# Kernel optimization log

Hardware: AMD Instinct MI355X
Metric: run time of the kernel (lower is better)

The kernel has to match this reference:

```python
import jax, jax.numpy as jnp
import numpy as np

B, N, D, S, H = 64, 4096, 256, 8, 256
ITERS = 3
EPS = 1e-8
SCALE = D ** -0.5


def _ln(x, g, b):
    m = jnp.mean(x, axis=-1, keepdims=True)
    v = jnp.mean((x - m) ** 2, axis=-1, keepdims=True)
    return (x - m) * jax.lax.rsqrt(v + 1e-5) * g + b


def setup_inputs() -> dict:
    key = jax.random.key(0)
    ks = jax.random.split(key, 12)
    s = 0.02
    return {
        'inputs': jax.random.normal(ks[0], (B, N, D), jnp.float32),
        'slot_noise': jax.random.normal(ks[1], (B, S, D), jnp.float32),
        'slots_mean': jax.random.normal(ks[2], (1, 1, D), jnp.float32),
        'slots_logvar': s * jax.random.normal(ks[3], (1, 1, D), jnp.float32),
        'Wq': s * jax.random.normal(ks[4], (D, D), jnp.float32),
        'bq': jnp.zeros((D,), jnp.float32),
        'Wk': s * jax.random.normal(ks[5], (D, D), jnp.float32),
        'bk': jnp.zeros((D,), jnp.float32),
        'Wv': s * jax.random.normal(ks[6], (D, D), jnp.float32),
        'bv': jnp.zeros((D,), jnp.float32),
        'W_ih': s * jax.random.normal(ks[7], (3 * D, D), jnp.float32),
        'b_ih': jnp.zeros((3 * D,), jnp.float32),
        'W_hh': s * jax.random.normal(ks[8], (3 * D, D), jnp.float32),
        'b_hh': jnp.zeros((3 * D,), jnp.float32),
        'W1': s * jax.random.normal(ks[9], (H, D), jnp.float32),
        'b1': jnp.zeros((H,), jnp.float32),
        'W2': s * jax.random.normal(ks[10], (D, H), jnp.float32),
        'b2': jnp.zeros((D,), jnp.float32),
        'g_in': jnp.ones((D,), jnp.float32),
        'bias_in': jnp.zeros((D,), jnp.float32),
        'g_slots': jnp.ones((D,), jnp.float32),
        'bias_slots': jnp.zeros((D,), jnp.float32),
        'g_ff': jnp.ones((D,), jnp.float32),
        'bias_ff': jnp.zeros((D,), jnp.float32),
    }


def reference(inputs, slot_noise, slots_mean, slots_logvar, Wq, bq, Wk, bk, Wv, bv,
              W_ih, b_ih, W_hh, b_hh, W1, b1, W2, b2,
              g_in, bias_in, g_slots, bias_slots, g_ff, bias_ff):
    # slot init: mean + exp(logvar) * noise  (exp(logvar) used as multiplier, as in source)
    slots = slots_mean + jnp.exp(slots_logvar) * slot_noise  # [B,S,D]
    x = _ln(inputs, g_in, bias_in)                            # [B,N,D]
    k = x @ Wk.T + bk
    v = x @ Wv.T + bv
    attn = None
    for _ in range(ITERS):
        slots_prev = slots
        sn = _ln(slots, g_slots, bias_slots)
        q = sn @ Wq.T + bq                                    # [B,S,D]
        dots = jnp.einsum('bid,bjd->bij', q, k) * SCALE       # [B,S,N]
        attn = jax.nn.softmax(dots, axis=1) + EPS             # softmax over slots, no renorm
        updates = jnp.einsum('bjd,bij->bid', v, attn)         # [B,S,D]
        # GRUCell (PyTorch convention)
        gi = updates @ W_ih.T + b_ih                          # [B,S,3D]
        gh = slots_prev @ W_hh.T + b_hh
        i_r, i_z, i_n = jnp.split(gi, 3, axis=-1)
        h_r, h_z, h_n = jnp.split(gh, 3, axis=-1)
        r = jax.nn.sigmoid(i_r + h_r)
        z = jax.nn.sigmoid(i_z + h_z)
        n = jnp.tanh(i_n + r * h_n)
        slots = (1.0 - z) * n + z * slots_prev
        # MLP residual
        sf = _ln(slots, g_ff, bias_ff)
        slots = slots + (jax.nn.relu(sf @ W1.T + b1) @ W2.T + b2)
    return (slots, attn)
```

## Files before the change

### kernel.cpp

```cpp
#include <hip/hip_runtime.h>

typedef unsigned short u16;
typedef __bf16 bf16x8 __attribute__((ext_vector_type(8)));
typedef float f32x4 __attribute__((ext_vector_type(4)));
typedef float f32x2 __attribute__((ext_vector_type(2)));

#define DEV static __device__ __forceinline__

DEV u16 f2bf(float f) {
    unsigned int u = __builtin_bit_cast(unsigned int, f);
    u += 0x7FFFu + ((u >> 16) & 1u);
    return (u16)(u >> 16);
}

DEV bf16x8 frag_ld(const u16* p) {
    return __builtin_bit_cast(bf16x8, *(const uint4*)p);
}

DEV float sigm(float x) { return 1.f / (1.f + __expf(-x)); }

DEV float blo(unsigned u) { return __builtin_bit_cast(float, u << 16); }
DEV float bhi(unsigned u) { return __builtin_bit_cast(float, u & 0xffff0000u); }
DEV f32x2 bf2(unsigned u) { return (f32x2){ blo(u), bhi(u) }; }

DEV int sw(int row, int colu16) { return row * 256 + (colu16 ^ ((row & 7) << 3)); }

DEV void gld16(const u16* g, u16* l) {
    __builtin_amdgcn_global_load_lds(
        (const __attribute__((address_space(1))) unsigned int*)g,
        (__attribute__((address_space(3))) unsigned int*)l, 16, 0, 0);
}

__global__ __launch_bounds__(256) void kSetupLN(
    const float* __restrict__ X, const float* __restrict__ gin, const float* __restrict__ bin,
    u16* __restrict__ XN,
    const float* __restrict__ noise, const float* __restrict__ mean,
    const float* __restrict__ logv, float* __restrict__ slots,
    const float* __restrict__ Wq, const float* __restrict__ Wk,
    const float* __restrict__ bq, const float* __restrict__ bk,
    float* __restrict__ Wqk, float* __restrict__ wbc,
    const float* __restrict__ Wv,  float* __restrict__ WvT,
    const float* __restrict__ Wih, float* __restrict__ WihT,
    const float* __restrict__ Whh, float* __restrict__ WhhT,
    const float* __restrict__ W1,  float* __restrict__ W1T,
    const float* __restrict__ W2,  float* __restrict__ W2T)
{
    __shared__ float tile[32][33];
    const int bid = blockIdx.x, t = threadIdx.x;
    if (bid < 2048) {
        const int w = t >> 6, lane = t & 63;
        const int c = lane << 2;
        const float4 g4 = *(const float4*)(gin + c);
        const float4 b4 = *(const float4*)(bin + c);
        const size_t r0 = (size_t)bid * 128 + (size_t)w * 32;
        #pragma unroll 4
        for (int i = 0; i < 32; ++i) {
            const float4 x = *(const float4*)(X + (r0 + i) * 256 + c);
            float s1 = x.x + x.y + x.z + x.w;
            float s2 = x.x * x.x + x.y * x.y + x.z * x.z + x.w * x.w;
            #pragma unroll
            for (int o = 32; o > 0; o >>= 1) { s1 += __shfl_xor(s1, o); s2 += __shfl_xor(s2, o); }
            const float mu = s1 * (1.f / 256.f);
            const float rs = rsqrtf(s2 * (1.f / 256.f) - mu * mu + 1e-5f);
            ushort4 pk;
            pk.x = f2bf((x.x - mu) * rs * g4.x + b4.x);
            pk.y = f2bf((x.y - mu) * rs * g4.y + b4.y);
            pk.z = f2bf((x.z - mu) * rs * g4.z + b4.z);
            pk.w = f2bf((x.w - mu) * rs * g4.w + b4.w);
            *(ushort4*)(XN + (r0 + i) * 256 + c) = pk;
        }
        return;
    }
    if (bid < 2560) {
        const int id = (bid - 2048) * 256 + t;
        const int d = id & 255;
        slots[id] = mean[d] + __expf(logv[d]) * noise[id];
        return;
    }
    if (bid < 2818) {
        const int a = bid - 2560, e = t;
        if (a < 256) {
            float acc = 0.f;
            for (int d = 0; d < 256; ++d) acc += Wq[(size_t)d * 256 + a] * Wk[(size_t)d * 256 + e];
            Wqk[(size_t)a * 256 + e] = acc;
        } else if (a == 256) {
            float acc = 0.f;
            for (int d = 0; d < 256; ++d) acc += bq[d] * Wk[(size_t)d * 256 + e];
            wbc[e] = acc;
        } else {
            float acc = 0.f;
            for (int d = 0; d < 256; ++d) acc += Wq[(size_t)d * 256 + e] * bk[d];
            wbc[256 + e] = acc;
            if (e == 0) {
                float c0 = 0.f;
                for (int d = 0; d < 256; ++d) c0 += bq[d] * bk[d];
                wbc[512] = c0;
            }
        }
        return;
    }
    const int rb = bid - 2818;
    const float* in; float* outp; int R, k;
    if (rb < 64)       { in = Wv;  outp = WvT;  R = 256; k = rb; }
    else if (rb < 256) { in = Wih; outp = WihT; R = 768; k = rb - 64; }
    else if (rb < 448) { in = Whh; outp = WhhT; R = 768; k = rb - 256; }
    else if (rb < 512) { in = W1;  outp = W1T;  R = 256; k = rb - 448; }
    else               { in = W2;  outp = W2T;  R = 256; k = rb - 512; }
    const int bx = k & 7, by = k >> 3;
    const int tx = t & 31, ty = t >> 5;
    const int c0 = bx * 32, r0 = by * 32;
    #pragma unroll
    for (int i = 0; i < 4; ++i)
        tile[ty + i * 8][tx] = in[(size_t)(r0 + ty + i * 8) * 256 + c0 + tx];
    __syncthreads();
    #pragma unroll
    for (int i = 0; i < 4; ++i)
        outp[(size_t)(c0 + ty + i * 8) * R + r0 + tx] = tile[tx][ty + i * 8];
}

__global__ __launch_bounds__(256) void kSn(
    const float* __restrict__ slots, const float* __restrict__ gs, const float* __restrict__ bs,
    const float* __restrict__ Wqk, const float* __restrict__ wbc,
    u16* __restrict__ qo, float* __restrict__ qc)
{
    __shared__ float SN[8][256];
    __shared__ float red2[4][8][64];
    const int t = threadIdx.x;
    const int b = blockIdx.y, seg = blockIdx.x;
    const int w = t >> 6, lane = t & 63;
    #pragma unroll
    for (int rr = 0; rr < 2; ++rr) {
        const int r = w * 2 + rr;
        const int c = lane * 4;
        const float4 x = *(const float4*)(slots + ((size_t)b * 8 + r) * 256 + c);
        float s1 = x.x + x.y + x.z + x.w;
        float s2 = x.x * x.x + x.y * x.y + x.z * x.z + x.w * x.w;
        #pragma unroll
        for (int o = 32; o > 0; o >>= 1) { s1 += __shfl_xor(s1, o); s2 += __shfl_xor(s2, o); }
        const float mu = s1 * (1.f / 256.f);
        const float rs = rsqrtf(s2 * (1.f / 256.f) - mu * mu + 1e-5f);
        const float4 g4 = *(const float4*)(gs + c);
        const float4 b4 = *(const float4*)(bs + c);
        SN[r][c + 0] = (x.x - mu) * rs * g4.x + b4.x;
        SN[r][c + 1] = (x.y - mu) * rs * g4.y + b4.y;
        SN[r][c + 2] = (x.z - mu) * rs * g4.z + b4.z;
        SN[r][c + 3] = (x.w - mu) * rs * g4.w + b4.w;
    }
    __syncthreads();
    const int c = seg * 64 + (t & 63);
    const int p = t >> 6;
    float acc[8] = {};
    #pragma unroll 4
    for (int d = p * 64; d < p * 64 + 64; ++d) {
        const float wq = Wqk[(size_t)d * 256 + c];
        #pragma unroll
        for (int r = 0; r < 8; ++r) acc[r] += wq * SN[r][d];
    }
    #pragma unroll
    for (int r = 0; r < 8; ++r) red2[p][r][t & 63] = acc[r];
    __syncthreads();
    const float bb = wbc[c];
    #pragma unroll
    for (int rr = t >> 6; rr < 8; rr += 4) {
        const float s = red2[0][rr][t & 63] + red2[1][rr][t & 63]
                      + red2[2][rr][t & 63] + red2[3][rr][t & 63];
        qo[((size_t)b * 16 + rr) * 256 + c] = f2bf((s + bb) * 0.0625f);
    }
    if (seg == 0) {
        const int r = t >> 5, l = t & 31;
        float a = 0.f;
        #pragma unroll
        for (int d8 = 0; d8 < 8; ++d8) a += SN[r][l * 8 + d8] * wbc[256 + l * 8 + d8];
        #pragma unroll
        for (int o = 16; o > 0; o >>= 1) a += __shfl_xor(a, o);
        if (l == 0) qc[(size_t)b * 8 + r] = 0.0625f * (a + wbc[512]);
    }
}

__global__ __launch_bounds__(256, 3) void kF(
    const u16* __restrict__ Q,
    const float* __restrict__ qcg,
    const u16* __restrict__ XN,
    float* __restrict__ attn_out,
    float* __restrict__ part,
    float* __restrict__ part2,
    int write_attn)
{
    __shared__ __align__(16) u16 stash[2 * 64 * 256];
    __shared__ __align__(16) float att32[64][8];
    const int tid = threadIdx.x;
    const int w = tid >> 6, lane = tid & 63;
    const int quad = lane >> 4, l16 = lane & 15;
    const int dsg = lane & 31, jg = lane >> 5;
    const int qb1 = (quad & 1) << 2;
    const int b = blockIdx.y, nt = blockIdx.x;
    const int j0 = nt << 8;
    const size_t rowbase = (size_t)b * 4096 + j0;
    const int srow = w * 16;

    const u16* qptr = Q + (size_t)b * 16 * 256;
    bf16x8 qfrag[8];
    #pragma unroll
    for (int k0 = 0; k0 < 8; ++k0)
        qfrag[k0] = frag_ld(qptr + l16 * 256 + k0 * 32 + quad * 8);

    float c8[8];
    #pragma unroll
    for (int i = 0; i < 8; ++i) c8[i] = qcg[(size_t)b * 8 + i];

    f32x2 acc2[8][4];
    #pragma unroll
    for (int i = 0; i < 8; ++i)
        #pragma unroll
        for (int k = 0; k < 4; ++k) acc2[i][k] = (f32x2){0.f, 0.f};
    float sacc[4] = {};

#define STAGE(ck, h)                                                          \
    {                                                                         \
        const u16* xb = XN + (rowbase + (ck) * 64) * 256;                     \
        u16* dst = stash + (h) * 16384;                                       \
        _Pragma("unroll")                                                     \
        for (int i = 0; i < 8; ++i) {                                         \
            const int il = i * 64 + lane;                                     \
            const int rloc = il >> 5;                                         \
            const int ug = (il & 31) ^ (rloc & 7);                            \
            gld16(xb + (size_t)(srow + rloc) * 256 + ug * 8,                  \
                  dst + ((srow << 5) + il) * 8);                              \
        }                                                                     \
    }

    STAGE(0, 0);
    for (int st = 0; st < 4; ++st) {
        if (st < 3) {
            STAGE(st + 1, (st + 1) & 1);
            asm volatile("s_waitcnt vmcnt(8)" ::: "memory");
        } else {
            asm volatile("s_waitcnt vmcnt(0)" ::: "memory");
        }
        const u16* sh = stash + (st & 1) * 16384;
        __builtin_amdgcn_s_setprio(1);

        f32x4 dacc = {};
        #pragma unroll
        for (int k0 = 0; k0 < 8; ++k0) {
            const bf16x8 bfr = frag_ld(sh + sw(srow + l16, k0 * 32 + quad * 8));
            dacc = __builtin_amdgcn_mfma_f32_16x16x32_bf16(qfrag[k0], bfr, dacc, 0, 0, 0);
        }
        {
            float v[8];
            #pragma unroll
            for (int r = 0; r < 4; ++r) {
                v[qb1 + r]       = dacc[r];
                v[(qb1 ^ 4) + r] = __shfl_xor(dacc[r], 16);
            }
            #pragma unroll
            for (int i = 0; i < 8; ++i) v[i] += c8[i];
            float m = v[0];
            #pragma unroll
            for (int i = 1; i < 8; ++i) m = fmaxf(m, v[i]);
            float s = 0.f;
            #pragma unroll
            for (int i = 0; i < 8; ++i) { v[i] = __expf(v[i] - m); s += v[i]; }
            const float inv = 1.f / s;
            if (quad < 2) {
                float4 av;
                av.x = v[qb1 + 0] * inv + 1e-8f;
                av.y = v[qb1 + 1] * inv + 1e-8f;
                av.z = v[qb1 + 2] * inv + 1e-8f;
                av.w = v[qb1 + 3] * inv + 1e-8f;
                sacc[0] += av.x; sacc[1] += av.y; sacc[2] += av.z; sacc[3] += av.w;
                *(float4*)&att32[srow + l16][qb1] = av;
                if (write_attn) {
                    const size_t jglob = j0 + st * 64 + srow + l16;
                    attn_out[((size_t)b * 8 + qb1 + 0) * 4096 + jglob] = av.x;
                    attn_out[((size_t)b * 8 + qb1 + 1) * 4096 + jglob] = av.y;
                    attn_out[((size_t)b * 8 + qb1 + 2) * 4096 + jglob] = av.z;
                    attn_out[((size_t)b * 8 + qb1 + 3) * 4096 + jglob] = av.w;
                }
            }
        }
        #pragma unroll
        for (int jj = 0; jj < 8; ++jj) {
            const int row = srow + jj * 2 + jg;
            const uint4 raw = *(const uint4*)(sh + sw(row, dsg * 8));
            const float4 a0 = *(const float4*)&att32[row][0];
            const float4 a1 = *(const float4*)&att32[row][4];
            f32x2 xf[4];
            xf[0] = bf2(raw.x); xf[1] = bf2(raw.y); xf[2] = bf2(raw.z); xf[3] = bf2(raw.w);
            const float av8[8] = {a0.x, a0.y, a0.z, a0.w, a1.x, a1.y, a1.z, a1.w};
            #pragma unroll
            for (int i = 0; i < 8; ++i) {
                const f32x2 aa = (f32x2){av8[i], av8[i]};
                #pragma unroll
                for (int k = 0; k < 4; ++k)
                    acc2[i][k] = aa * xf[k] + acc2[i][k];
            }
        }
        __builtin_amdgcn_s_setprio(0);
    }
#undef STAGE

    #pragma unroll
    for (int i = 0; i < 8; ++i)
        #pragma unroll
        for (int k = 0; k < 4; ++k) {
            acc2[i][k][0] += __shfl_xor(acc2[i][k][0], 32);
            acc2[i][k][1] += __shfl_xor(acc2[i][k][1], 32);
        }
    #pragma unroll
    for (int r = 0; r < 4; ++r)
        #pragma unroll
        for (int o = 1; o < 16; o <<= 1) sacc[r] += __shfl_xor(sacc[r], o);

    __syncthreads();
    float* usred = (float*)stash;
    float* sred2 = (float*)att32;
    if (jg == 0) {
        #pragma unroll
        for (int i = 0; i < 8; ++i) {
            float4 lo, hi;
            lo.x = acc2[i][0][0]; lo.y = acc2[i][0][1]; lo.z = acc2[i][1][0]; lo.w = acc2[i][1][1];
            hi.x = acc2[i][2][0]; hi.y = acc2[i][2][1]; hi.z = acc2[i][3][0]; hi.w = acc2[i][3][1];
            *(float4*)&usred[(w * 8 + i) * 256 + dsg * 8]     = lo;
            *(float4*)&usred[(w * 8 + i) * 256 + dsg * 8 + 4] = hi;
        }
    }
    if (l16 == 0 && quad < 2) {
        #pragma unroll
        for (int r = 0; r < 4; ++r) sred2[(w * 2 + quad) * 4 + r] = sacc[r];
    }
    __syncthreads();
    const size_t pb = ((size_t)nt * 64 + b) * 8;
    #pragma unroll
    for (int i = 0; i < 8; ++i) {
        const float s = usred[(0 * 8 + i) * 256 + tid] + usred[(1 * 8 + i) * 256 + tid]
                      + usred[(2 * 8 + i) * 256 + tid] + usred[(3 * 8 + i) * 256 + tid];
        part[(pb + i) * 256 + tid] = s;
    }
    if (tid < 8) {
        const int q = tid >> 2, r = tid & 3;
        part2[pb + tid] = sred2[(0 * 2 + q) * 4 + r] + sred2[(1 * 2 + q) * 4 + r]
                        + sred2[(2 * 2 + q) * 4 + r] + sred2[(3 * 2 + q) * 4 + r];
    }
}

__global__ __launch_bounds__(256) void kB3(
    const float* __restrict__ part, const float* __restrict__ part2,
    const float* __restrict__ WvT, const float* __restrict__ bv,
    const float* __restrict__ sl_in,
    const float* __restrict__ WihT, const float* __restrict__ bih,
    const float* __restrict__ WhhT, const float* __restrict__ bhh,
    const float* __restrict__ W1T, const float* __restrict__ b1,
    const float* __restrict__ W2T, const float* __restrict__ b2,
    const float* __restrict__ gf, const float* __restrict__ bff,
    float* __restrict__ sl_out)
{
    __shared__ float Ul[2][256], Sl[2][256];
    __shared__ float red[2][4][6][256];
    __shared__ float SNl[2][256];
    __shared__ float cw[2][2][4];
    __shared__ float Ssl[2];
    const int t = threadIdx.x;
    const int kp = t >> 6, c = t & 63;
    const int row0 = blockIdx.x * 2;

    #pragma unroll
    for (int r = 0; r < 2; ++r) {
        const int row = row0 + r;
        const int b = row >> 3, s = row & 7;
        float ua0 = 0.f, ua1 = 0.f;
        #pragma unroll
        for (int u = 0; u < 16; u += 2) {
            ua0 += part[(((size_t)u * 64 + b) * 8 + s) * 256 + t];
            ua1 += part[(((size_t)(u + 1) * 64 + b) * 8 + s) * 256 + t];
        }
        Ul[r][t] = ua0 + ua1;
        Sl[r][t] = sl_in[(size_t)row * 256 + t];
    }
    if (t < 2) {
        const int row = row0 + t;
        const int b = row >> 3, s = row & 7;
        float ss = 0.f;
        #pragma unroll
        for (int u = 0; u < 16; ++u) ss += part2[((size_t)u * 64 + b) * 8 + s];
        Ssl[t] = ss;
    }
    __syncthreads();

    {
        float va[2][4] = {};
        #pragma unroll 4
        for (int dd = 0; dd < 64; ++dd) {
            const int d = kp * 64 + dd;
            const float* wr = WvT + (size_t)d * 256;
            const float u0 = Ul[0][d], u1 = Ul[1][d];
            #pragma unroll
            for (int cg = 0; cg < 4; ++cg) {
                const float wv = wr[cg * 64 + c];
                va[0][cg] += wv * u0;
                va[1][cg] += wv * u1;
            }
        }
        #pragma unroll
        for (int r = 0; r < 2; ++r)
            #pragma unroll
            for (int cg = 0; cg < 4; ++cg)
                red[r][kp][0][cg * 64 + c] = va[r][cg];
    }
    __syncthreads();
    const float bvt = bv[t];
    float upd2[2];
    #pragma unroll
    for (int r = 0; r < 2; ++r)
        upd2[r] = red[r][0][0][t] + red[r][1][0][t] + red[r][2][0][t] + red[r][3][0][t]
                + Ssl[r] * bvt;
    __syncthreads();
    #pragma unroll
    for (int r = 0; r < 2; ++r) Ul[r][t] = upd2[r];
    __syncthreads();

    float ga[2][4][6] = {};
    #pragma unroll 2
    for (int dd = 0; dd < 64; ++dd) {
        const int d = kp * 64 + dd;
        const float* wi = WihT + (size_t)d * 768;
        const float* wh = WhhT + (size_t)d * 768;
        const float u0 = Ul[0][d], u1 = Ul[1][d];
        const float s0 = Sl[0][d], s1 = Sl[1][d];
        #pragma unroll
        for (int cg = 0; cg < 4; ++cg) {
            const int t2 = cg * 64 + c;
            const float wa = wi[t2], wb = wi[256 + t2], wc = wi[512 + t2];
            const float wd = wh[t2], we = wh[256 + t2], wf = wh[512 + t2];
            ga[0][cg][0] += wa * u0; ga[0][cg][1] += wb * u0; ga[0][cg][2] += wc * u0;
            ga[0][cg][3] += wd * s0; ga[0][cg][4] += we * s0; ga[0][cg][5] += wf * s0;
            ga[1][cg][0] += wa * u1; ga[1][cg][1] += wb * u1; ga[1][cg][2] += wc * u1;
            ga[1][cg][3] += wd * s1; ga[1][cg][4] += we * s1; ga[1][cg][5] += wf * s1;
        }
    }
    #pragma unroll
    for (int r = 0; r < 2; ++r)
        #pragma unroll
        for (int cg = 0; cg < 4; ++cg)
            #pragma unroll
            for (int g = 0; g < 6; ++g)
                red[r][kp][g][cg * 64 + c] = ga[r][cg][g];
    __syncthreads();

    const float b_ir = bih[t], b_iz = bih[256 + t], b_in = bih[512 + t];
    const float b_hr = bhh[t], b_hz = bhh[256 + t], b_hn = bhh[512 + t];
    float hnew[2];
    #pragma unroll
    for (int r = 0; r < 2; ++r) {
        float s6[6];
        #pragma unroll
        for (int g = 0; g < 6; ++g)
            s6[g] = red[r][0][g][t] + red[r][1][g][t] + red[r][2][g][t] + red[r][3][g][t];
        const float rg = sigm(s6[0] + b_ir + s6[3] + b_hr);
        const float zg = sigm(s6[1] + b_iz + s6[4] + b_hz);
        const float ng = tanhf(s6[2] + b_in + rg * (s6[5] + b_hn));
        hnew[r] = (1.f - zg) * ng + zg * Sl[r][t];
    }
    #pragma unroll
    for (int r = 0; r < 2; ++r) {
        float s1 = hnew[r], s2 = hnew[r] * hnew[r];
        #pragma unroll
        for (int o = 32; o > 0; o >>= 1) { s1 += __shfl_xor(s1, o); s2 += __shfl_xor(s2, o); }
        if (c == 0) { cw[r][0][kp] = s1; cw[r][1][kp] = s2; }
    }
    __syncthreads();
    const float gft = gf[t], bfft = bff[t];
    #pragma unroll
    for (int r = 0; r < 2; ++r) {
        const float s1 = cw[r][0][0] + cw[r][0][1] + cw[r][0][2] + cw[r][0][3];
        const float s2 = cw[r][1][0] + cw[r][1][1] + cw[r][1][2] + cw[r][1][3];
        const float mu = s1 * (1.f / 256.f);
        const float rs = rsqrtf(s2 * (1.f / 256.f) - mu * mu + 1e-5f);
        SNl[r][t] = (hnew[r] - mu) * rs * gft + bfft;
    }
    __syncthreads();

    {
        float m1[2][4] = {};
        #pragma unroll 4
        for (int dd = 0; dd < 64; ++dd) {
            const int d = kp * 64 + dd;
            const float* wr = W1T + (size_t)d * 256;
            const float n0 = SNl[0][d], n1 = SNl[1][d];
            #pragma unroll
            for (int cg = 0; cg < 4; ++cg) {
                const float wv = wr[cg * 64 + c];
                m1[0][cg] += wv * n0;
                m1[1][cg] += wv * n1;
            }
        }
        #pragma unroll
        for (int r = 0; r < 2; ++r)
            #pragma unroll
            for (int cg = 0; cg < 4; ++cg)
                red[r][kp][0][cg * 64 + c] = m1[r][cg];
    }
    __syncthreads();
    const float b1t = b1[t];
    float h1v[2];
    #pragma unroll
    for (int r = 0; r < 2; ++r)
        h1v[r] = fmaxf(red[r][0][0][t] + red[r][1][0][t] + red[r][2][0][t] + red[r][3][0][t]
                       + b1t, 0.f);
    __syncthreads();
    #pragma unroll
    for (int r = 0; r < 2; ++r) SNl[r][t] = h1v[r];
    __syncthreads();
    {
        float m2[2][4] = {};
        #pragma unroll 4
        for (int dd = 0; dd < 64; ++dd) {
            const int d = kp * 64 + dd;
            const float* wr = W2T + (size_t)d * 256;
            const float x0 = SNl[0][d], x1 = SNl[1][d];
            #pragma unroll
            for (int cg = 0; cg < 4; ++cg) {
                const float wv = wr[cg * 64 + c];
                m2[0][cg] += wv * x0;
                m2[1][cg] += wv * x1;
            }
        }
        #pragma unroll
        for (int r = 0; r < 2; ++r)
            #pragma unroll
            for (int cg = 0; cg < 4; ++cg)
                red[r][kp][1][cg * 64 + c] = m2[r][cg];
    }
    __syncthreads();
    const float b2t = b2[t];
    #pragma unroll
    for (int r = 0; r < 2; ++r) {
        const float o = red[r][0][1][t] + red[r][1][1][t] + red[r][2][1][t] + red[r][3][1][t];
        sl_out[(size_t)(row0 + r) * 256 + t] = hnew[r] + o + b2t;
    }
}

extern "C" void kernel_launch(void* const* d_in, const int* in_sizes, int n_in,
                              void* d_out, int out_size, void* d_ws, size_t ws_size,
                              hipStream_t stream) {
    const float* inputs = (const float*)d_in[0];
    const float* noise  = (const float*)d_in[1];
    const float* smean  = (const float*)d_in[2];
    const float* slogv  = (const float*)d_in[3];
    const float* Wq  = (const float*)d_in[4];
    const float* bq  = (const float*)d_in[5];
    const float* Wk  = (const float*)d_in[6];
    const float* bk  = (const float*)d_in[7];
    const float* Wv  = (const float*)d_in[8];
    const float* bv  = (const float*)d_in[9];
    const float* Wih = (const float*)d_in[10];
    const float* bih = (const float*)d_in[11];
    const float* Whh = (const float*)d_in[12];
    const float* bhh = (const float*)d_in[13];
    const float* W1  = (const float*)d_in[14];
    const float* b1  = (const float*)d_in[15];
    const float* W2  = (const float*)d_in[16];
    const float* b2  = (const float*)d_in[17];
    const float* gin = (const float*)d_in[18];
    const float* bin = (const float*)d_in[19];
    const float* gs  = (const float*)d_in[20];
    const float* bs  = (const float*)d_in[21];
    const float* gf  = (const float*)d_in[22];
    const float* bff = (const float*)d_in[23];

    char* ws = (char*)d_ws;
    u16*  XNw    = (u16*)(ws);
    u16*  qw     = (u16*)(ws + 134217728ull);
    float* slots = (float*)(ws + 134742016ull);
    float* Wqkw  = (float*)(ws + 135266304ull);
    float* wbc   = (float*)(ws + 135528448ull);
    float* qcw   = (float*)(ws + 135532544ull);
    float* WvT   = (float*)(ws + 135536640ull);
    float* WihT  = (float*)(ws + 135798784ull);
    float* WhhT  = (float*)(ws + 136585216ull);
    float* W1T   = (float*)(ws + 137371648ull);
    float* W2T   = (float*)(ws + 137633792ull);
    float* partw = (float*)(ws + 137895936ull);
    float* part2w= (float*)(ws + 146284544ull);

    float* out = (float*)d_out;
    float* attn_out = out + 131072;

    kSetupLN<<<3394, 256, 0, stream>>>(inputs, gin, bin, XNw,
                                       noise, smean, slogv, slots,
                                       Wq, Wk, bq, bk, Wqkw, wbc,
                                       Wv, WvT, Wih, WihT, Whh, WhhT, W1, W1T, W2, W2T);
    for (int it = 0; it < 3; ++it) {
        kSn<<<dim3(4, 64), 256, 0, stream>>>(slots, gs, bs, Wqkw, wbc, qw, qcw);
        kF<<<dim3(16, 64), 256, 0, stream>>>(qw, qcw, XNw, attn_out, partw, part2w, it == 2);
        kB3<<<256, 256, 0, stream>>>(partw, part2w, WvT, bv, slots,
                                     WihT, bih, WhhT, bhh, W1T, b1, W2T, b2, gf, bff,
                                     (it == 2) ? out : slots);
    }
}
```

Before: 667.2 us.

## Fuse next-iteration slot LayerNorm and query projection into GRU/MLP kernel

The per-iteration kSn launch, which normalizes slots and projects them through the fused Wq·Wk matrix, now runs only once before the loop. For later iterations the same LayerNorm, projection, bias and per-row constant are computed at the tail of kB3, from slot values still held in registers. This removes two kernel launches and a round trip of the slots through global memory. In exchange kB3 gets longer and has more shared-memory syncs, with only 256 blocks doing the projection work. Small unroll pragmas were also added to the setup Wqk loops.

After: 679.3 us. No clear change (+1.8%).

```diff
diff --git a/kernel.cpp b/kernel.cpp
--- a/kernel.cpp
+++ b/kernel.cpp
@@ -81,14 +81,17 @@
         const int a = bid - 2560, e = t;
         if (a < 256) {
             float acc = 0.f;
+            #pragma unroll 4
             for (int d = 0; d < 256; ++d) acc += Wq[(size_t)d * 256 + a] * Wk[(size_t)d * 256 + e];
             Wqk[(size_t)a * 256 + e] = acc;
         } else if (a == 256) {
             float acc = 0.f;
+            #pragma unroll 4
             for (int d = 0; d < 256; ++d) acc += bq[d] * Wk[(size_t)d * 256 + e];
             wbc[e] = acc;
         } else {
             float acc = 0.f;
+            #pragma unroll 4
             for (int d = 0; d < 256; ++d) acc += Wq[(size_t)d * 256 + e] * bk[d];
             wbc[256 + e] = acc;
             if (e == 0) {
@@ -353,7 +356,10 @@
     const float* __restrict__ W1T, const float* __restrict__ b1,
     const float* __restrict__ W2T, const float* __restrict__ b2,
     const float* __restrict__ gf, const float* __restrict__ bff,
-    float* __restrict__ sl_out)
+    const float* __restrict__ Wqk, const float* __restrict__ wbc,
+    const float* __restrict__ gs, const float* __restrict__ bs,
+    u16* __restrict__ qo, float* __restrict__ qc,
+    float* __restrict__ sl_out, int emit_q)
 {
     __shared__ float Ul[2][256], Sl[2][256];
     __shared__ float red[2][4][6][256];
@@ -533,10 +539,79 @@
     }
     __syncthreads();
     const float b2t = b2[t];
+    float outv[2];
     #pragma unroll
     for (int r = 0; r < 2; ++r) {
         const float o = red[r][0][1][t] + red[r][1][1][t] + red[r][2][1][t] + red[r][3][1][t];
-        sl_out[(size_t)(row0 + r) * 256 + t] = hnew[r] + o + b2t;
+        outv[r] = hnew[r] + o + b2t;
+        sl_out[(size_t)(row0 + r) * 256 + t] = outv[r];
+    }
+    if (!emit_q) return;
+
+    __syncthreads();
+    #pragma unroll
+    for (int r = 0; r < 2; ++r) {
+        float s1 = outv[r], s2 = outv[r] * outv[r];
+        #pragma unroll
+        for (int o = 32; o > 0; o >>= 1) { s1 += __shfl_xor(s1, o); s2 += __shfl_xor(s2, o); }
+        if (c == 0) { cw[r][0][kp] = s1; cw[r][1][kp] = s2; }
+    }
+    __syncthreads();
+    float snq[2];
+    const float gst = gs[t], bst = bs[t];
+    #pragma unroll
+    for (int r = 0; r < 2; ++r) {
+        const float s1 = cw[r][0][0] + cw[r][0][1] + cw[r][0][2] + cw[r][0][3];
+        const float s2 = cw[r][1][0] + cw[r][1][1] + cw[r][1][2] + cw[r][1][3];
+        const float mu = s1 * (1.f / 256.f);
+        const float rs = rsqrtf(s2 * (1.f / 256.f) - mu * mu + 1e-5f);
+        snq[r] = (outv[r] - mu) * rs * gst + bst;
+    }
+    __syncthreads();
+    Ul[0][t] = snq[0];
+    Ul[1][t] = snq[1];
+    __syncthreads();
+    {
+        float qa[2][4] = {};
+        #pragma unroll 4
+        for (int dd = 0; dd < 64; ++dd) {
+            const int d = kp * 64 + dd;
+            const float* wr = Wqk + (size_t)d * 256;
+            const float u0 = Ul[0][d], u1 = Ul[1][d];
+            #pragma unroll
+            for (int cg = 0; cg < 4; ++cg) {
+                const float wv = wr[cg * 64 + c];
+                qa[0][cg] += wv * u0;
+                qa[1][cg] += wv * u1;
+            }
+        }
+        #pragma unroll
+        for (int r = 0; r < 2; ++r)
+            #pragma unroll
+            for (int cg = 0; cg < 4; ++cg)
+                red[r][kp][0][cg * 64 + c] = qa[r][cg];
+    }
+    __syncthreads();
+    const float bqk = wbc[t];
+    #pragma unroll
+    for (int r = 0; r < 2; ++r) {
+        const float qs = red[r][0][0][t] + red[r][1][0][t] + red[r][2][0][t] + red[r][3][0][t];
+        const int row = row0 + r, bb = row >> 3, ss = row & 7;
+        qo[((size_t)bb * 16 + ss) * 256 + t] = f2bf((qs + bqk) * 0.0625f);
+    }
+    const float wbt = wbc[256 + t];
+    #pragma unroll
+    for (int r = 0; r < 2; ++r) {
+        float p = snq[r] * wbt;
+        #pragma unroll
+        for (int o = 32; o > 0; o >>= 1) p += __shfl_xor(p, o);
+        if (c == 0) cw[r][0][kp] = p;
+    }
+    __syncthreads();
+    if (t < 2) {
+        const int row = row0 + t, bb = row >> 3, ss = row & 7;
+        qc[(size_t)bb * 8 + ss] = 0.0625f * (cw[t][0][0] + cw[t][0][1] + cw[t][0][2]
+                                             + cw[t][0][3] + wbc[512]);
     }
 }
 
@@ -590,11 +665,12 @@
                                        noise, smean, slogv, slots,
                                        Wq, Wk, bq, bk, Wqkw, wbc,
                                        Wv, WvT, Wih, WihT, Whh, WhhT, W1, W1T, W2, W2T);
+    kSn<<<dim3(4, 64), 256, 0, stream>>>(slots, gs, bs, Wqkw, wbc, qw, qcw);
     for (int it = 0; it < 3; ++it) {
-        kSn<<<dim3(4, 64), 256, 0, stream>>>(slots, gs, bs, Wqkw, wbc, qw, qcw);
         kF<<<dim3(16, 64), 256, 0, stream>>>(qw, qcw, XNw, attn_out, partw, part2w, it == 2);
         kB3<<<256, 256, 0, stream>>>(partw, part2w, WvT, bv, slots,
                                      WihT, bih, WhhT, bhh, W1T, b1, W2T, b2, gf, bff,
-                                     (it == 2) ? out : slots);
-    }
-}
+                                     Wqkw, wbc, gs, bs, qw, qcw,
+                                     (it == 2) ? out : slots, it < 2);
+    }
+}
```
